# Kernel tuning notes

Measured on AMD Instinct MI355X. Metric: run time of the kernel, lower is better.

## Reference

```python
import jax, jax.numpy as jnp
import numpy as np

DIM = 768
HEADS = 12
HEAD_DIM = DIM // HEADS
R = 8            # LoRA rank (cfg.EXPERT_LOW_RANK)
E = 4            # number of routed LoRA experts in proj (cfg.EXPERT_NUM)
LORA_SCALE = 1.0 / R   # lora_alpha(=1) / r
TOPK_T_PCT = 50  # cfg.topk_tempalte (percent)
TOPK_S_PCT = 25  # cfg.topk_search (percent)
B = 4
N_M = 256        # template / memory tokens
N_S = 1024       # search tokens
N = N_M + N_S
MEM = 1280       # cached memory kv length


def setup_inputs() -> dict:
    key = jax.random.key(0)
    ks = jax.random.split(key, 24)
    g = lambda i, shape: jax.random.normal(ks[i], shape, dtype=jnp.float32) * 0.02
    return dict(
        x=jax.random.normal(ks[0], (B, N, DIM), dtype=jnp.float32),
        id_total=jax.random.normal(ks[1], (B, N_M, DIM), dtype=jnp.float32),
        mem_k=jax.random.normal(ks[2], (B, HEADS, MEM, HEAD_DIM), dtype=jnp.float32),
        mem_v=jax.random.normal(ks[3], (B, HEADS, MEM, HEAD_DIM), dtype=jnp.float32),
        W_qkv=g(4, (3 * DIM, DIM)), b_qkv=g(5, (3 * DIM,)),
        qkv_A=g(6, (3, R, DIM)), qkv_B=g(7, (3, DIM, R)),
        W_proj=g(8, (DIM, DIM)), b_proj=g(9, (DIM,)),
        route_W=g(10, (E, DIM)), proj_A=g(11, (E, R, DIM)), proj_B=g(12, (E, DIM, R)),
        W_idk=g(13, (HEADS, DIM)), b_idk=g(14, (HEADS,)),
        idk_A=g(15, (R, DIM)), idk_B=g(16, (HEADS, R)),
        W_idv=g(17, (DIM, DIM)), b_idv=g(18, (DIM,)),
        idv_A=g(19, (R, DIM)), idv_B=g(20, (DIM, R)),
    )


def _lora1(x, W, b, A, Bm):
    # LinearExperts with lora_num=1: softmax over a single route logit == 1.0
    return x @ W.T + b + ((x @ A.T) @ Bm.T) * LORA_SCALE


def _softmax_w_top(att, top):
    # topk values (sorted desc) -> stable exp relative to the max -> normalize -> scatter
    vals, idx = jax.lax.top_k(att, top)
    e = jnp.exp(vals - vals[..., :1])
    e = e / jnp.sum(e, axis=-1, keepdims=True)
    b, h, q, _ = att.shape
    bi = jnp.arange(b)[:, None, None, None]
    hi = jnp.arange(h)[None, :, None, None]
    qi = jnp.arange(q)[None, None, :, None]
    return jnp.zeros_like(att).at[bi, hi, qi, idx].set(e.astype(att.dtype))


def _forward(x, id_total, mem_k, mem_v, W_qkv, b_qkv, qkv_A, qkv_B,
             W_proj, b_proj, route_W, proj_A, proj_B,
             W_idk, b_idk, idk_A, idk_B, W_idv, b_idv, idv_A, idv_B):
    Bb, Nn, C = x.shape
    Nm = id_total.shape[1]
    Ns = Nn - Nm
    H, D = HEADS, C // HEADS
    # MergedLinear qkv: dense + per-group (q,k,v) LoRA
    low = jnp.einsum('bnc,grc->bngr', x, qkv_A)
    lora = (jnp.einsum('bngr,gcr->bngc', low, qkv_B) * LORA_SCALE).reshape(Bb, Nn, 3 * C)
    qkv = (x @ W_qkv.T + b_qkv + lora).reshape(Bb, Nn, 3, H, D).transpose(2, 0, 3, 1, 4)
    q, k, v = qkv[0], qkv[1], qkv[2]          # each (B,H,N,D)
    k_m, v_m, v_s = k[:, :, :Nm], v[:, :, :Nm], v[:, :, Nm:]
    # memory-token ID gating (id_add=True path)
    ID_K = _lora1(id_total, W_idk, b_idk, idk_A, idk_B)   # (B,Nm,H)
    ID_V = _lora1(id_total, W_idv, b_idv, idv_A, idv_B)   # (B,Nm,C)
    k_m_id = k_m * (1.0 + jnp.tanh(ID_K)).transpose(0, 2, 1)[..., None]
    v_m_flat = v_m.transpose(0, 2, 1, 3).reshape(Bb, Nm, C) + ID_V
    v_m_id = v_m_flat.reshape(Bb, Nm, H, D).transpose(0, 2, 1, 3)
    v_add_id = jnp.concatenate([v_m_id, v_s], axis=2)
    q = q * (D ** -0.5)
    q_m, q_s = q[:, :, :Nm], q[:, :, Nm:]
    # template self-attention with topk softmax
    attn_m = q_m @ k_m_id.transpose(0, 1, 3, 2)           # (B,H,Nm,Nm)
    attn_m = _softmax_w_top(attn_m, int(TOPK_T_PCT / 100 * Nm))
    x_m = (attn_m @ v_m_id).transpose(0, 2, 1, 3).reshape(Bb, Nm, C)
    # search attention over [mem_k, k] (k is the ORIGINAL un-gated key, as in torch)
    k_full = jnp.concatenate([mem_k, k], axis=2)
    v_full = jnp.concatenate([mem_v, v_add_id], axis=2)
    attn_s = q_s @ k_full.transpose(0, 1, 3, 2)           # (B,H,Ns,MEM+N)
    attn_s = _softmax_w_top(attn_s, int(TOPK_S_PCT / 100 * k_full.shape[2]))
    x_s = (attn_s @ v_full).transpose(0, 2, 1, 3).reshape(Bb, Ns, C)
    xo = jnp.concatenate([x_m, x_s], axis=1)
    # LinearExperts proj: dense + softmax-routed LoRA experts
    route = jax.nn.softmax((xo @ route_W.T).astype(jnp.float32), axis=-1).astype(xo.dtype)
    low = jnp.einsum('bnc,erc->bner', xo, proj_A)
    up = jnp.einsum('bner,ecr->bnec', low, proj_B)
    out = xo @ W_proj.T + b_proj + jnp.einsum('bne,bnec->bnc', route, up) * LORA_SCALE
    return out, k_m_id, v_m_id


def reference(x, id_total, mem_k, mem_v, W_qkv, b_qkv, qkv_A, qkv_B,
              W_proj, b_proj, route_W, proj_A, proj_B,
              W_idk, b_idk, idk_A, idk_B, W_idv, b_idv, idv_A, idv_B):
    return _forward(x, id_total, mem_k, mem_v, W_qkv, b_qkv, qkv_A, qkv_B,
                    W_proj, b_proj, route_W, proj_A, proj_B,
                    W_idk, b_idk, idk_A, idk_B, W_idv, b_idv, idv_A, idv_B)
```

## Files before the change

### kernel.cpp

```cpp
#include <hip/hip_runtime.h>
#include <cstddef>

#define Bq    4
#define Hh    12
#define Dd    64
#define NNtok 1280
#define DIMc  768
#define KAUG  800
#define NBH   48

typedef __attribute__((ext_vector_type(8))) short bf16x8;
typedef __attribute__((ext_vector_type(4))) float f32x4;

static const size_t OVb   = 0;
static const size_t OXO   = 3932160;
static const size_t OQL   = 7864320;
static const size_t OIDK  = 7987200;
static const size_t OIDV  = 7999488;
static const size_t OLK   = 8785920;
static const size_t OLV   = 8794112;
static const size_t ORD   = 8802304;
static const size_t OPL   = 8822784;
static const size_t OQH   = 8986624;
static const size_t OKFH  = 10952704;
static const size_t OVTH  = 14884864;
static const size_t OKMH  = 18817024;
static const size_t OVMTH = 19210240;
static const size_t OAa   = 19603456;
static const size_t OWa   = 21651456;
static const size_t OWa2  = 22573056;

static const size_t KMID_OFF = 3932160;
static const size_t VMID_OFF = 4718592;

__device__ __forceinline__ unsigned int pk_bf16(float a, float b) {
  unsigned int ua = __float_as_uint(a), ub = __float_as_uint(b);
  ua += 0x7fffu + ((ua >> 16) & 1u);
  ub += 0x7fffu + ((ub >> 16) & 1u);
  return (ua >> 16) | (ub & 0xffff0000u);
}
__device__ __forceinline__ unsigned short bf16_1(float a) {
  unsigned int ua = __float_as_uint(a);
  ua += 0x7fffu + ((ua >> 16) & 1u);
  return (unsigned short)(ua >> 16);
}
__device__ __forceinline__ float bf2f(unsigned int h) {
  return __uint_as_float(h << 16);
}

__global__ __launch_bounds__(256) void prep(
    const float* __restrict__ mem_k, const float* __restrict__ mem_v,
    const float* __restrict__ W_qkv, const float* __restrict__ qkvB,
    const float* __restrict__ W_proj, const float* __restrict__ projB,
    unsigned short* __restrict__ kfh, unsigned short* __restrict__ vth,
    unsigned short* __restrict__ Wa, unsigned short* __restrict__ Wa2)
{
  __shared__ float tl[64][65];
  const int blk = blockIdx.x, t = threadIdx.x;
  if (blk < 1920) {
    size_t idx = ((size_t)blk * 256 + t) * 8;
    int bh = (int)(idx / 81920);
    int r  = (int)(idx % 81920);
    const float* s = mem_k + (size_t)bh * 81920 + r;
    float4 a = *(const float4*)s;
    float4 b = *(const float4*)(s + 4);
    unsigned int* dp = (unsigned int*)(kfh + (size_t)bh * 163840 + r);
    dp[0] = pk_bf16(a.x, a.y); dp[1] = pk_bf16(a.z, a.w);
    dp[2] = pk_bf16(b.x, b.y); dp[3] = pk_bf16(b.z, b.w);
  } else if (blk < 2880) {
    int b2 = blk - 1920;
    int bh = b2 / 20, t0 = (b2 % 20) * 64;
    const float* sb = mem_v + (size_t)bh * 81920 + (size_t)t0 * 64;
#pragma unroll
    for (int p = 0; p < 4; ++p) {
      int flat = p * 256 + t;
      int r = flat >> 4, c4 = (flat & 15) << 2;
      float4 v = *(const float4*)(sb + r * 64 + c4);
      tl[r][c4 + 0] = v.x; tl[r][c4 + 1] = v.y;
      tl[r][c4 + 2] = v.z; tl[r][c4 + 3] = v.w;
    }
    __syncthreads();
    unsigned short* db = vth + (size_t)bh * 163840 + t0;
#pragma unroll
    for (int p = 0; p < 8; ++p) {
      int flat = p * 256 + t;
      int d = flat >> 5, u = flat & 31;
      *(unsigned int*)(db + (size_t)d * 2560 + 2 * u) = pk_bf16(tl[2 * u][d], tl[2 * u + 1][d]);
    }
  } else if (blk < 6480) {
    int idx = (blk - 2880) * 256 + t;
    int row = idx / 400, c = (idx % 400) * 2;
    float a, b;
    if (c < 768) {
      a = W_qkv[(size_t)row * 768 + c]; b = W_qkv[(size_t)row * 768 + c + 1];
    } else {
      int g = row / 768, jj = row % 768;
      int e0 = c - 768, e1 = e0 + 1;
      a = (e0 < 24 && (e0 >> 3) == g) ? qkvB[(size_t)g * 6144 + jj * 8 + (e0 & 7)] * 0.125f : 0.f;
      b = (e1 < 24 && (e1 >> 3) == g) ? qkvB[(size_t)g * 6144 + jj * 8 + (e1 & 7)] * 0.125f : 0.f;
    }
    *(unsigned int*)(Wa + (size_t)row * KAUG + c) = pk_bf16(a, b);
  } else {
    int idx = (blk - 6480) * 256 + t;
    int row = idx / 400, c = (idx % 400) * 2;
    float a, b;
    if (c < 768) {
      a = W_proj[(size_t)row * 768 + c]; b = W_proj[(size_t)row * 768 + c + 1];
    } else {
      int e0 = c - 768, e1 = e0 + 1;
      a = projB[(size_t)(e0 >> 3) * 6144 + row * 8 + (e0 & 7)];
      b = projB[(size_t)(e1 >> 3) * 6144 + row * 8 + (e1 & 7)];
    }
    *(unsigned int*)(Wa2 + (size_t)row * KAUG + c) = pk_bf16(a, b);
  }
}

__global__ __launch_bounds__(256) void dots_fused(
    const float* __restrict__ x, const float* __restrict__ qkvA,
    float* __restrict__ qlow,
    const float* __restrict__ id_tot, const float* __restrict__ idkA,
    const float* __restrict__ idvA, float* __restrict__ lowk,
    float* __restrict__ lowv)
{
  const int wv = threadIdx.x >> 6, ln = threadIdx.x & 63;
  if (blockIdx.x < 1280) {
    size_t row = (size_t)blockIdx.x * 4 + wv;
    const float* s = x + row * DIMc;
    float xr[12];
#pragma unroll
    for (int i = 0; i < 12; ++i) xr[i] = s[ln + i * 64];
    float p[24];
#pragma unroll
    for (int o = 0; o < 24; ++o) {
      const float* m = qkvA + (size_t)o * DIMc;
      float acc = 0.f;
#pragma unroll
      for (int i = 0; i < 12; ++i) acc += xr[i] * m[ln + i * 64];
      p[o] = acc;
    }
#pragma unroll
    for (int off = 32; off; off >>= 1)
#pragma unroll
      for (int o = 0; o < 24; ++o) p[o] += __shfl_xor(p[o], off, 64);
    if (ln == 0) {
#pragma unroll
      for (int o = 0; o < 24; ++o) qlow[row * 24 + o] = p[o];
    }
  } else {
    size_t row = (size_t)(blockIdx.x - 1280) * 4 + wv;
    const float* s = id_tot + row * DIMc;
    float xr[12];
#pragma unroll
    for (int i = 0; i < 12; ++i) xr[i] = s[ln + i * 64];
    float p[16];
#pragma unroll
    for (int o = 0; o < 8; ++o) {
      const float* m1 = idkA + (size_t)o * DIMc;
      const float* m2 = idvA + (size_t)o * DIMc;
      float a1 = 0.f, a2 = 0.f;
#pragma unroll
      for (int i = 0; i < 12; ++i) {
        a1 += xr[i] * m1[ln + i * 64];
        a2 += xr[i] * m2[ln + i * 64];
      }
      p[o] = a1; p[8 + o] = a2;
    }
#pragma unroll
    for (int off = 32; off; off >>= 1)
#pragma unroll
      for (int o = 0; o < 16; ++o) p[o] += __shfl_xor(p[o], off, 64);
    if (ln == 0) {
#pragma unroll
      for (int o = 0; o < 8; ++o) { lowk[row * 8 + o] = p[o]; lowv[row * 8 + o] = p[8 + o]; }
    }
  }
}

__global__ __launch_bounds__(256) void dot_rp(
    const float* __restrict__ xo, const float* __restrict__ routeW,
    const float* __restrict__ projA, float* __restrict__ rd,
    float* __restrict__ plow)
{
  int wv = threadIdx.x >> 6, ln = threadIdx.x & 63;
  size_t row = (size_t)blockIdx.x * 4 + wv;
  const float* s = xo + row * DIMc;
  float xr[12];
#pragma unroll
  for (int i = 0; i < 12; ++i) xr[i] = s[ln + i * 64];
  float pr[4];
#pragma unroll
  for (int o = 0; o < 4; ++o) {
    const float* m = routeW + (size_t)o * DIMc;
    float acc = 0.f;
#pragma unroll
    for (int i = 0; i < 12; ++i) acc += xr[i] * m[ln + i * 64];
    pr[o] = acc;
  }
  float pl[32];
#pragma unroll
  for (int o = 0; o < 32; ++o) {
    const float* m = projA + (size_t)o * DIMc;
    float acc = 0.f;
#pragma unroll
    for (int i = 0; i < 12; ++i) acc += xr[i] * m[ln + i * 64];
    pl[o] = acc;
  }
#pragma unroll
  for (int off = 32; off; off >>= 1) {
#pragma unroll
    for (int o = 0; o < 4; ++o) pr[o] += __shfl_xor(pr[o], off, 64);
#pragma unroll
    for (int o = 0; o < 32; ++o) pl[o] += __shfl_xor(pl[o], off, 64);
  }
  if (ln == 0) {
#pragma unroll
    for (int o = 0; o < 4; ++o) rd[row * 4 + o] = pr[o];
#pragma unroll
    for (int o = 0; o < 32; ++o) plow[row * 32 + o] = pl[o];
  }
}

__global__ __launch_bounds__(256) void idv_idk(
    const float* __restrict__ id_tot,
    const float* __restrict__ W_idv, const float* __restrict__ b_idv,
    const float* __restrict__ lowv, const float* __restrict__ idv_B,
    float* __restrict__ IDV,
    const float* __restrict__ W_idk, const float* __restrict__ b_idk,
    const float* __restrict__ lowk, const float* __restrict__ idk_B,
    float* __restrict__ IDK)
{
  __shared__ alignas(16) float As[16][68];
  __shared__ alignas(16) float Bs[16][68];
  const int blk = blockIdx.x, t = threadIdx.x;
  if (blk < 192) {
    const int tx = t & 15, ty = t >> 4;
    const int bn = (blk % 12) * 64, bm = (blk / 12) * 64;
    const int am = t >> 2, ak = (t & 3) << 2;
    float acc[4][4] = {};
    for (int k0 = 0; k0 < 768; k0 += 16) {
      float4 av = *(const float4*)(id_tot + (size_t)(bm + am) * 768 + k0 + ak);
      float4 bv = *(const float4*)(W_idv + (size_t)(bn + am) * 768 + k0 + ak);
      As[ak + 0][am] = av.x; As[ak + 1][am] = av.y; As[ak + 2][am] = av.z; As[ak + 3][am] = av.w;
      Bs[ak + 0][am] = bv.x; Bs[ak + 1][am] = bv.y; Bs[ak + 2][am] = bv.z; Bs[ak + 3][am] = bv.w;
      __syncthreads();
#pragma unroll
      for (int kk = 0; kk < 16; ++kk) {
        float4 a4 = *(const float4*)&As[kk][ty << 2];
        float4 b4 = *(const float4*)&Bs[kk][tx << 2];
        float ar[4] = { a4.x, a4.y, a4.z, a4.w };
        float br[4] = { b4.x, b4.y, b4.z, b4.w };
#pragma unroll
        for (int i = 0; i < 4; ++i)
#pragma unroll
          for (int j = 0; j < 4; ++j) acc[i][j] += ar[i] * br[j];
      }
      __syncthreads();
    }
#pragma unroll
    for (int i = 0; i < 4; ++i) {
      int mg = bm + (ty << 2) + i;
#pragma unroll
      for (int j = 0; j < 4; ++j) {
        int col = bn + (tx << 2) + j;
        float v = acc[i][j] + b_idv[col];
        float lo = 0.f;
#pragma unroll
        for (int r = 0; r < 8; ++r) lo += lowv[(size_t)mg * 8 + r] * idv_B[(size_t)col * 8 + r];
        IDV[(size_t)mg * 768 + col] = v + lo * 0.125f;
      }
    }
  } else {
    int wv = t >> 6, ln = t & 63;
    size_t row = (size_t)(blk - 192) * 4 + wv;
    const float* s = id_tot + row * DIMc;
    float xr[12];
#pragma unroll
    for (int i = 0; i < 12; ++i) xr[i] = s[ln + i * 64];
    float p[12];
#pragma unroll
    for (int h = 0; h < 12; ++h) {
      const float* m = W_idk + (size_t)h * DIMc;
      float acc = 0.f;
#pragma unroll
      for (int i = 0; i < 12; ++i) acc += xr[i] * m[ln + i * 64];
      p[h] = acc;
    }
#pragma unroll
    for (int off = 32; off; off >>= 1)
#pragma unroll
      for (int h = 0; h < 12; ++h) p[h] += __shfl_xor(p[h], off, 64);
    if (ln == 0) {
#pragma unroll
      for (int h = 0; h < 12; ++h) {
        float lo = 0.f;
#pragma unroll
        for (int r = 0; r < 8; ++r) lo += lowk[row * 8 + r] * idk_B[h * 8 + r];
        IDK[row * Hh + h] = 1.f + tanhf(p[h] + b_idk[h] + lo * 0.125f);
      }
    }
  }
}

__global__ __launch_bounds__(256) void fixup_kernel(
    float* __restrict__ vb, const float* __restrict__ IDK,
    const float* __restrict__ IDV, float* __restrict__ kmid,
    float* __restrict__ vmid, unsigned short* __restrict__ kmh)
{
  int e = blockIdx.x * 256 + threadIdx.x;
  int d  = e & 63;
  int r1 = e >> 6;
  int tt = r1 & 255;
  int r2 = r1 >> 8;
  int h  = r2 % Hh;
  int b  = r2 / Hh;
  float km = kmid[e] * IDK[(size_t)(b * 256 + tt) * Hh + h];
  kmid[e] = km;
  kmh[e] = bf16_1(km);
  size_t src = ((size_t)(b * Hh + h) * NNtok + tt) * Dd + d;
  float vv = vb[src] + IDV[(size_t)(b * 256 + tt) * DIMc + h * 64 + d];
  vb[src] = vv;
  vmid[e] = vv;
}

__global__ __launch_bounds__(256) void transpose_post(
    const float* __restrict__ vb, unsigned short* __restrict__ vth,
    unsigned short* __restrict__ vmth)
{
  __shared__ float tl[64][65];
  const int blk = blockIdx.x, t = threadIdx.x;
  int bh, t0, dstCols, colOfs;
  unsigned short* dstp;
  size_t dstBh;
  if (blk < 960) { bh = blk / 20; t0 = (blk % 20) * 64; dstp = vth; dstBh = 163840; dstCols = 2560; colOfs = 1280; }
  else { int b2 = blk - 960; bh = b2 / 4; t0 = (b2 % 4) * 64; dstp = vmth; dstBh = 16384; dstCols = 256; colOfs = 0; }
  const float* sb = vb + (size_t)bh * 81920 + (size_t)t0 * 64;
#pragma unroll
  for (int p = 0; p < 4; ++p) {
    int flat = p * 256 + t;
    int r = flat >> 4, c4 = (flat & 15) << 2;
    float4 v = *(const float4*)(sb + r * 64 + c4);
    tl[r][c4 + 0] = v.x; tl[r][c4 + 1] = v.y;
    tl[r][c4 + 2] = v.z; tl[r][c4 + 3] = v.w;
  }
  __syncthreads();
  unsigned short* db = dstp + (size_t)bh * dstBh + colOfs + t0;
#pragma unroll
  for (int p = 0; p < 8; ++p) {
    int flat = p * 256 + t;
    int d = flat >> 5, u = flat & 31;
    *(unsigned int*)(db + (size_t)d * dstCols + 2 * u) = pk_bf16(tl[2 * u][d], tl[2 * u + 1][d]);
  }
}

__global__ __launch_bounds__(256) void cast_pack(
    const float* __restrict__ mainp, const float* __restrict__ extra,
    unsigned short* __restrict__ dst, int extraN)
{
  int idx = blockIdx.x * 256 + threadIdx.x;
  int row = idx / 100, c8 = (idx % 100) * 8;
  unsigned int w[4];
  if (c8 < 768) {
    const float* s = mainp + (size_t)row * 768 + c8;
    float4 a = *(const float4*)s;
    float4 b = *(const float4*)(s + 4);
    w[0] = pk_bf16(a.x, a.y); w[1] = pk_bf16(a.z, a.w);
    w[2] = pk_bf16(b.x, b.y); w[3] = pk_bf16(b.z, b.w);
  } else {
    float v[8];
#pragma unroll
    for (int j = 0; j < 8; ++j) {
      int e = c8 - 768 + j;
      v[j] = (e < extraN) ? extra[(size_t)row * extraN + e] : 0.f;
    }
    w[0] = pk_bf16(v[0], v[1]); w[1] = pk_bf16(v[2], v[3]);
    w[2] = pk_bf16(v[4], v[5]); w[3] = pk_bf16(v[6], v[7]);
  }
  *(uint4*)(dst + (size_t)row * KAUG + c8) = make_uint4(w[0], w[1], w[2], w[3]);
}

__global__ __launch_bounds__(256) void cast_pack_proj(
    const float* __restrict__ xo, const float* __restrict__ rd,
    const float* __restrict__ plow, unsigned short* __restrict__ dst)
{
  int idx = blockIdx.x * 256 + threadIdx.x;
  int row = idx / 100, c8 = (idx % 100) * 8;
  unsigned int w[4];
  if (c8 < 768) {
    const float* s = xo + (size_t)row * 768 + c8;
    float4 a = *(const float4*)s;
    float4 b = *(const float4*)(s + 4);
    w[0] = pk_bf16(a.x, a.y); w[1] = pk_bf16(a.z, a.w);
    w[2] = pk_bf16(b.x, b.y); w[3] = pk_bf16(b.z, b.w);
  } else {
    float l0 = rd[row * 4 + 0], l1 = rd[row * 4 + 1], l2 = rd[row * 4 + 2], l3 = rd[row * 4 + 3];
    float m = fmaxf(fmaxf(l0, l1), fmaxf(l2, l3));
    float e0 = __expf(l0 - m), e1 = __expf(l1 - m), e2 = __expf(l2 - m), e3 = __expf(l3 - m);
    float inv = 0.125f / (e0 + e1 + e2 + e3);
    float rt[4] = { e0 * inv, e1 * inv, e2 * inv, e3 * inv };
    float v[8];
#pragma unroll
    for (int j = 0; j < 8; ++j) {
      int e = c8 - 768 + j;
      v[j] = (e < 32) ? rt[e >> 3] * plow[(size_t)row * 32 + e] : 0.f;
    }
    w[0] = pk_bf16(v[0], v[1]); w[1] = pk_bf16(v[2], v[3]);
    w[2] = pk_bf16(v[4], v[5]); w[3] = pk_bf16(v[6], v[7]);
  }
  *(uint4*)(dst + (size_t)row * KAUG + c8) = make_uint4(w[0], w[1], w[2], w[3]);
}

__global__ __launch_bounds__(256) void gemm_mfma(
    const unsigned short* __restrict__ A, const unsigned short* __restrict__ W,
    const float* __restrict__ bias, int mode, float* __restrict__ dst,
    unsigned short* __restrict__ qh, float* __restrict__ kmid,
    float* __restrict__ vb, unsigned short* __restrict__ kfh)
{
  const int t = threadIdx.x, w = t >> 6, l = t & 63;
  const int m = l & 15, quad = l >> 4;
  const int bm = blockIdx.y * 128 + (w >> 1) * 64;
  const int bn = blockIdx.x * 128 + (w & 1) * 64;
  f32x4 acc[4][4] = {};
  const unsigned short* Ab = A + (size_t)(bm + m) * KAUG;
  const unsigned short* Wb = W + (size_t)(bn + m) * KAUG;
  for (int kk = 0; kk < KAUG; kk += 32) {
    bf16x8 af[4], bf[4];
#pragma unroll
    for (int i = 0; i < 4; ++i) af[i] = *(const bf16x8*)(Ab + (size_t)i * 16 * KAUG + kk + quad * 8);
#pragma unroll
    for (int j = 0; j < 4; ++j) bf[j] = *(const bf16x8*)(Wb + (size_t)j * 16 * KAUG + kk + quad * 8);
#pragma unroll
    for (int i = 0; i < 4; ++i)
#pragma unroll
      for (int j = 0; j < 4; ++j)
        acc[i][j] = __builtin_amdgcn_mfma_f32_16x16x32_bf16(af[i], bf[j], acc[i][j], 0, 0, 0);
  }

  float bj[4];
#pragma unroll
  for (int j = 0; j < 4; ++j) bj[j] = bias[bn + j * 16 + m];

  if (mode == 2) {
#pragma unroll
    for (int i = 0; i < 4; ++i)
#pragma unroll
      for (int r = 0; r < 4; ++r) {
        int row = bm + i * 16 + quad * 4 + r;
#pragma unroll
        for (int j = 0; j < 4; ++j)
          dst[(size_t)row * 768 + bn + j * 16 + m] = acc[i][j][r] + bj[j];
      }
    return;
  }
  int g = (blockIdx.x * 128) / DIMc;
#pragma unroll
  for (int j = 0; j < 4; ++j) {
    int col = bn + j * 16 + m;
    int jj = col - g * DIMc, hh = jj >> 6, d = jj & 63;
#pragma unroll
    for (int i = 0; i < 4; ++i)
#pragma unroll
      for (int r = 0; r < 4; ++r) {
        int row = bm + i * 16 + quad * 4 + r;
        int bb = row / NNtok, tt = row % NNtok;
        float v = acc[i][j][r] + bj[j];
        if (g == 0) {
          qh[((size_t)(bb * Hh + hh) * NNtok + tt) * Dd + d] = bf16_1(v * 0.125f);
        } else if (g == 1) {
          kfh[((size_t)(bb * Hh + hh) * 2560 + 1280 + tt) * Dd + d] = bf16_1(v);
          if (tt < 256) kmid[((size_t)(bb * Hh + hh) * 256 + tt) * Dd + d] = v;
        } else {
          vb[((size_t)(bb * Hh + hh) * NNtok + tt) * Dd + d] = v;
        }
      }
  }
}

__device__ __forceinline__ void radix_sel(
    unsigned int* hist, int l, int& kk, int& ceq, unsigned int& bin)
{
  unsigned int h0 = hist[4 * l + 0], h1 = hist[4 * l + 1],
               h2 = hist[4 * l + 2], h3 = hist[4 * l + 3];
  unsigned int s3 = h3, s2 = h2 + s3, s1 = h1 + s2, s0 = h0 + s1;
  unsigned int tsum = s0;
#pragma unroll
  for (int off = 1; off < 64; off <<= 1) {
    unsigned int other = __shfl(tsum, l + off, 64);
    tsum += (l + off < 64) ? other : 0u;
  }
  unsigned int T = tsum - s0;
  unsigned int Sv0 = T + s0, Sv1 = T + s1, Sv2 = T + s2, Sv3 = T + s3, Sv4 = T;
  int fb = -1, fkk = 0, fceq = 0;
  unsigned int ukk = (unsigned int)kk;
  if (Sv0 >= ukk && Sv1 < ukk) { fb = 4 * l + 0; fkk = (int)(ukk - Sv1); fceq = (int)(Sv0 - Sv1); }
  if (Sv1 >= ukk && Sv2 < ukk) { fb = 4 * l + 1; fkk = (int)(ukk - Sv2); fceq = (int)(Sv1 - Sv2); }
  if (Sv2 >= ukk && Sv3 < ukk) { fb = 4 * l + 2; fkk = (int)(ukk - Sv3); fceq = (int)(Sv2 - Sv3); }
  if (Sv3 >= ukk && Sv4 < ukk) { fb = 4 * l + 3; fkk = (int)(ukk - Sv4); fceq = (int)(Sv3 - Sv4); }
  unsigned long long mb = __ballot(fb >= 0);
  int src = __ffsll(mb) - 1;
  bin = (unsigned int)__shfl(fb, src, 64);
  kk  = __shfl(fkk, src, 64);
  ceq = __shfl(fceq, src, 64);
}

template<int NK>
__global__ __launch_bounds__(256, 3) void attn_mfma7(
    const unsigned short* __restrict__ qh,
    const unsigned short* __restrict__ kf,
    const unsigned short* __restrict__ vt,
    int TK, int qrow0, float* __restrict__ xo, int nofs)
{
  constexpr int SCP = NK + 8;
  constexpr int W = NK / 128;
  constexpr int NRB = (NK == 256) ? 32 : 128;
  __shared__ alignas(16) unsigned short sc16[8][SCP];
  __shared__ unsigned int hist8[8][256];
  __shared__ float wavemax[4][8];
  __shared__ float rowinv[8];

  const int t = threadIdx.x, w = t >> 6, l = t & 63;
  const int xcd  = (int)blockIdx.x & 7;
  const int slot = (int)blockIdx.x >> 3;
  const int bh   = xcd * (NBH / 8) + slot / NRB;
  const int rb   = slot % NRB;
  const int b = bh / Hh, h = bh % Hh;
  const int qbase = qrow0 + rb * 8;
  const int m = l & 15, quad = l >> 4;

  bf16x8 aq0 = {0,0,0,0,0,0,0,0}, aq1 = {0,0,0,0,0,0,0,0};
  if (m < 8) {
    const unsigned short* qp = qh + ((size_t)bh * NNtok + qbase + m) * Dd + quad * 8;
    aq0 = *(const bf16x8*)qp;
    aq1 = *(const bf16x8*)(qp + 32);
  }
  float mx[4] = { -3.0e38f, -3.0e38f, -3.0e38f, -3.0e38f };
  constexpr int ITA = NK / 64;
  constexpr int GA = (ITA >= 4) ? 4 : ITA;
  const unsigned short* kpA = kf + (size_t)bh * NK * Dd + (size_t)(w * 16 + m) * Dd + quad * 8;
  bf16x8 kbuf[2][GA][2];
#pragma unroll
  for (int i = 0; i < GA; ++i) {
    kbuf[0][i][0] = *(const bf16x8*)(kpA + (size_t)i * 64 * Dd);
    kbuf[0][i][1] = *(const bf16x8*)(kpA + (size_t)i * 64 * Dd + 32);
  }
  int ab = 0;
  for (int g0 = 0; g0 < ITA; g0 += GA) {
    if (g0 + GA < ITA) {
#pragma unroll
      for (int i = 0; i < GA; ++i) {
        kbuf[1 - ab][i][0] = *(const bf16x8*)(kpA + (size_t)(g0 + GA + i) * 64 * Dd);
        kbuf[1 - ab][i][1] = *(const bf16x8*)(kpA + (size_t)(g0 + GA + i) * 64 * Dd + 32);
      }
    }
#pragma unroll
    for (int i = 0; i < GA; ++i) {
      int n0 = w * 16 + (g0 + i) * 64;
      f32x4 acc = {0.f, 0.f, 0.f, 0.f};
      acc = __builtin_amdgcn_mfma_f32_16x16x32_bf16(aq0, kbuf[ab][i][0], acc, 0, 0, 0);
      acc = __builtin_amdgcn_mfma_f32_16x16x32_bf16(aq1, kbuf[ab][i][1], acc, 0, 0, 0);
      if (quad < 2) {
#pragma unroll
        for (int r = 0; r < 4; ++r) {
          float v = acc[r];
          mx[r] = fmaxf(mx[r], v);
          sc16[quad * 4 + r][n0 + m] = bf16_1(v);
        }
      }
    }
    ab ^= 1;
  }
#pragma unroll
  for (int off = 1; off < 16; off <<= 1)
#pragma unroll
    for (int r = 0; r < 4; ++r) mx[r] = fmaxf(mx[r], __shfl_xor(mx[r], off, 64));
  if (l == 0) {
#pragma unroll
    for (int r = 0; r < 4; ++r) wavemax[w][r] = mx[r];
  }
  if (l == 16) {
#pragma unroll
    for (int r = 0; r < 4; ++r) wavemax[w][4 + r] = mx[r];
  }
  __syncthreads();

  const int r0i = w * 2, r1i = w * 2 + 1;
  unsigned int* sp0 = (unsigned int*)&sc16[r0i][0];
  unsigned int* sp1 = (unsigned int*)&sc16[r1i][0];
  unsigned int* h0 = hist8[r0i];
  unsigned int* h1 = hist8[r1i];
#pragma unroll
  for (int z = 0; z < 4; ++z) { h0[l + z * 64] = 0u; h1[l + z * 64] = 0u; }
  unsigned int kw0[W], kw1[W];
#pragma unroll
  for (int j = 0; j < W; ++j) {
    unsigned int v0 = sp0[j * 64 + l];
    unsigned int v1 = sp1[j * 64 + l];
    v0 = v0 ^ (((v0 >> 15) & 0x00010001u) * 0x7fffu + 0x80008000u);
    v1 = v1 ^ (((v1 >> 15) & 0x00010001u) * 0x7fffu + 0x80008000u);
    kw0[j] = v0; kw1[j] = v1;
    atomicAdd(&h0[(v0 >> 8) & 255u], 1u);
    atomicAdd(&h0[v0 >> 24], 1u);
    atomicAdd(&h1[(v1 >> 8) & 255u], 1u);
    atomicAdd(&h1[v1 >> 24], 1u);
  }
  int kk0 = TK, kk1 = TK;
  int ceq0s, ceq1s;
  unsigned int bin0, bin1;
  radix_sel(h0, l, kk0, ceq0s, bin0);
  radix_sel(h1, l, kk1, ceq1s, bin1);
  const unsigned int pf0 = bin0 << 8, pf1 = bin1 << 8;
  (void)ceq0s; (void)ceq1s;

  auto finish = [&](unsigned int* kwp, unsigned int prefix, int kk, int row,
                    unsigned int* sp) {
    unsigned int* hist = hist8[row];
#pragma unroll
    for (int z = 0; z < 4; ++z) hist[l + z * 64] = 0u;
    const unsigned int pfx8 = prefix >> 8;
#pragma unroll
    for (int j = 0; j < W; ++j) {
      unsigned int k2 = kwp[j];
      unsigned int lo = k2 & 0xFFFFu, hi = k2 >> 16;
      if ((lo >> 8) == pfx8) atomicAdd(&hist[lo & 255u], 1u);
      if ((hi >> 8) == pfx8) atomicAdd(&hist[hi & 255u], 1u);
    }
    unsigned int b2;
    int ceq = 0;
    radix_sel(hist, l, kk, ceq, b2);
    const unsigned int Tkey = prefix | b2;
    const int need = kk;
    if (need < ceq) {
      int seen = 0;
      unsigned long long below = (1ull << l) - 1ull;
#pragma unroll
      for (int j = 0; j < W; ++j) {
        unsigned int k2 = kwp[j];
        bool eq0 = ((k2 & 0xFFFFu) == Tkey);
        bool eq1 = ((k2 >> 16) == Tkey);
        unsigned long long m0 = __ballot(eq0), m1 = __ballot(eq1);
        int bfr = __popcll(m0 & below) + __popcll(m1 & below);
        if (eq0 && (seen + bfr) >= need) kwp[j] &= 0xFFFF0000u;
        if (eq1 && (seen + bfr + (eq0 ? 1 : 0)) >= need) kwp[j] &= 0x0000FFFFu;
        seen += __popcll(m0) + __popcll(m1);
      }
    }
    float rm = fmaxf(fmaxf(wavemax[0][row], wavemax[1][row]),
                     fmaxf(wavemax[2][row], wavemax[3][row]));
    float sum = 0.f;
#pragma unroll
    for (int j = 0; j < W; ++j) {
      unsigned int k2 = kwp[j];
      unsigned int lo = k2 & 0xFFFFu, hi = k2 >> 16;
      unsigned int mm = ((~k2 >> 15) & 0x00010001u) * 0x7fffu + 0x80008000u;
      unsigned int o2 = k2 ^ mm;
      float v0 = bf2f(o2 & 0xFFFFu);
      float v1 = bf2f(o2 >> 16);
      float w0 = (lo >= Tkey) ? __expf(v0 - rm) : 0.f;
      float w1 = (hi >= Tkey) ? __expf(v1 - rm) : 0.f;
      sp[j * 64 + l] = pk_bf16(w0, w1);
      sum += w0 + w1;
    }
#pragma unroll
    for (int off = 32; off; off >>= 1) sum += __shfl_xor(sum, off, 64);
    if (l == 0) rowinv[row] = 1.f / sum;
  };
  finish(kw0, pf0, kk0, r0i, sp0);
  finish(kw1, pf1, kk1, r1i, sp1);
  __syncthreads();

  constexpr int ITD = NK / 32;
  constexpr int GD = (ITD >= 4) ? 4 : ITD;
  const unsigned short* vrow = vt + (size_t)bh * Dd * NK + (size_t)(w * 16 + m) * NK + quad * 8;
  f32x4 o = {0.f, 0.f, 0.f, 0.f};
  const bf16x8 zz = {0,0,0,0,0,0,0,0};
  bf16x8 vbuf[2][GD], wbuf[2][GD];
#pragma unroll
  for (int i = 0; i < GD; ++i) {
    vbuf[0][i] = *(const bf16x8*)(vrow + i * 32);
    wbuf[0][i] = (m < 8) ? *(const bf16x8*)&sc16[m][i * 32 + quad * 8] : zz;
  }
  int db = 0;
  for (int g0 = 0; g0 < ITD; g0 += GD) {
    if (g0 + GD < ITD) {
#pragma unroll
      for (int i = 0; i < GD; ++i) {
        vbuf[1 - db][i] = *(const bf16x8*)(vrow + (g0 + GD + i) * 32);
        wbuf[1 - db][i] = (m < 8) ? *(const bf16x8*)&sc16[m][(g0 + GD + i) * 32 + quad * 8] : zz;
      }
    }
#pragma unroll
    for (int i = 0; i < GD; ++i)
      o = __builtin_amdgcn_mfma_f32_16x16x32_bf16(wbuf[db][i], vbuf[db][i], o, 0, 0, 0);
    db ^= 1;
  }
  if (quad < 2) {
#pragma unroll
    for (int r = 0; r < 4; ++r) {
      int row = quad * 4 + r;
      int n = nofs + rb * 8 + row;
      xo[((size_t)b * NNtok + n) * DIMc + h * 64 + w * 16 + m] = o[r] * rowinv[row];
    }
  }
}

extern "C" void kernel_launch(void* const* d_in, const int* in_sizes, int n_in,
                              void* d_out, int out_size, void* d_ws, size_t ws_size,
                              hipStream_t stream)
{
  const float* x       = (const float*)d_in[0];
  const float* id_tot  = (const float*)d_in[1];
  const float* mem_k   = (const float*)d_in[2];
  const float* mem_v   = (const float*)d_in[3];
  const float* W_qkv   = (const float*)d_in[4];
  const float* b_qkv   = (const float*)d_in[5];
  const float* qkv_A   = (const float*)d_in[6];
  const float* qkv_B   = (const float*)d_in[7];
  const float* W_proj  = (const float*)d_in[8];
  const float* b_proj  = (const float*)d_in[9];
  const float* route_W = (const float*)d_in[10];
  const float* proj_A  = (const float*)d_in[11];
  const float* proj_B  = (const float*)d_in[12];
  const float* W_idk   = (const float*)d_in[13];
  const float* b_idk   = (const float*)d_in[14];
  const float* idk_A   = (const float*)d_in[15];
  const float* idk_B   = (const float*)d_in[16];
  const float* W_idv   = (const float*)d_in[17];
  const float* b_idv   = (const float*)d_in[18];
  const float* idv_A   = (const float*)d_in[19];
  const float* idv_B   = (const float*)d_in[20];

  float* ws   = (float*)d_ws;
  float* vb   = ws + OVb;
  float* xo   = ws + OXO;
  float* qlow = ws + OQL;
  float* IDK  = ws + OIDK;
  float* IDV  = ws + OIDV;
  float* lowk = ws + OLK;
  float* lowv = ws + OLV;
  float* rd   = ws + ORD;
  float* plow = ws + OPL;
  unsigned short* qh   = (unsigned short*)(ws + OQH);
  unsigned short* kfh  = (unsigned short*)(ws + OKFH);
  unsigned short* vth  = (unsigned short*)(ws + OVTH);
  unsigned short* kmh  = (unsigned short*)(ws + OKMH);
  unsigned short* vmth = (unsigned short*)(ws + OVMTH);
  unsigned short* Aa   = (unsigned short*)(ws + OAa);
  unsigned short* Wa   = (unsigned short*)(ws + OWa);
  unsigned short* Wa2  = (unsigned short*)(ws + OWa2);

  float* out  = (float*)d_out;
  float* kmid = out + KMID_OFF;
  float* vmid = out + VMID_OFF;

  prep<<<7680, 256, 0, stream>>>(mem_k, mem_v, W_qkv, qkv_B, W_proj, proj_B,
                                 kfh, vth, Wa, Wa2);

  dots_fused<<<1536, 256, 0, stream>>>(x, qkv_A, qlow,
                                       id_tot, idk_A, idv_A, lowk, lowv);

  cast_pack<<<2000, 256, 0, stream>>>(x, qlow, Aa, 24);
  gemm_mfma<<<dim3(18, 40), 256, 0, stream>>>(Aa, Wa, b_qkv, 0, nullptr,
                                              qh, kmid, vb, kfh);
  idv_idk<<<448, 256, 0, stream>>>(id_tot, W_idv, b_idv, lowv, idv_B, IDV,
                                   W_idk, b_idk, lowk, idk_B, IDK);
  fixup_kernel<<<3072, 256, 0, stream>>>(vb, IDK, IDV, kmid, vmid, kmh);

  transpose_post<<<1152, 256, 0, stream>>>(vb, vth, vmth);

  attn_mfma7<256><<<1536, 256, 0, stream>>>(qh, kmh, vmth, 128, 0, xo, 0);
  attn_mfma7<2560><<<6144, 256, 0, stream>>>(qh, kfh, vth, 640, 256, xo, 256);

  dot_rp<<<1280, 256, 0, stream>>>(xo, route_W, proj_A, rd, plow);
  cast_pack_proj<<<2000, 256, 0, stream>>>(xo, rd, plow, Aa);
  gemm_mfma<<<dim3(6, 40), 256, 0, stream>>>(Aa, Wa2, b_proj, 2, out,
                                             nullptr, nullptr, nullptr, nullptr);
}
```

Before: 907.2 us.

## Fuse prep with low-rank dots, merge attention launches, fuse routing into proj pack

The low-rank dot products for qkv/id LoRA become extra block ranges of the prep kernel. The two attention launches (memory part and full-context part) become one launch that dispatches on block index, with shared buffers sized for the larger variant. The route/proj_A dot kernel is folded into cast_pack_proj, so the softmax routing and LoRA low values stay in registers instead of going through workspace. The aim is fewer launches, less tail idle between them, and one fewer global round trip. The cost is that the short-context attention blocks now reserve the larger shared allocation, and each wave in the proj pack writes its row serially.

```diff
diff --git a/kernel.cpp b/kernel.cpp
--- a/kernel.cpp
+++ b/kernel.cpp
@@ -19,8 +19,6 @@
 static const size_t OIDV  = 7999488;
 static const size_t OLK   = 8785920;
 static const size_t OLV   = 8794112;
-static const size_t ORD   = 8802304;
-static const size_t OPL   = 8822784;
 static const size_t OQH   = 8986624;
 static const size_t OKFH  = 10952704;
 static const size_t OVTH  = 14884864;
@@ -53,7 +51,12 @@
     const float* __restrict__ W_qkv, const float* __restrict__ qkvB,
     const float* __restrict__ W_proj, const float* __restrict__ projB,
     unsigned short* __restrict__ kfh, unsigned short* __restrict__ vth,
-    unsigned short* __restrict__ Wa, unsigned short* __restrict__ Wa2)
+    unsigned short* __restrict__ Wa, unsigned short* __restrict__ Wa2,
+    const float* __restrict__ x, const float* __restrict__ qkvA,
+    float* __restrict__ qlow,
+    const float* __restrict__ id_tot, const float* __restrict__ idkA,
+    const float* __restrict__ idvA, float* __restrict__ lowk,
+    float* __restrict__ lowv)
 {
   __shared__ float tl[64][65];
   const int blk = blockIdx.x, t = threadIdx.x;
@@ -100,7 +103,7 @@
       b = (e1 < 24 && (e1 >> 3) == g) ? qkvB[(size_t)g * 6144 + jj * 8 + (e1 & 7)] * 0.125f : 0.f;
     }
     *(unsigned int*)(Wa + (size_t)row * KAUG + c) = pk_bf16(a, b);
-  } else {
+  } else if (blk < 7680) {
     int idx = (blk - 6480) * 256 + t;
     int row = idx / 400, c = (idx % 400) * 2;
     float a, b;
@@ -112,111 +115,60 @@
       b = projB[(size_t)(e1 >> 3) * 6144 + row * 8 + (e1 & 7)];
     }
     *(unsigned int*)(Wa2 + (size_t)row * KAUG + c) = pk_bf16(a, b);
-  }
-}
-
-__global__ __launch_bounds__(256) void dots_fused(
-    const float* __restrict__ x, const float* __restrict__ qkvA,
-    float* __restrict__ qlow,
-    const float* __restrict__ id_tot, const float* __restrict__ idkA,
-    const float* __restrict__ idvA, float* __restrict__ lowk,
-    float* __restrict__ lowv)
-{
-  const int wv = threadIdx.x >> 6, ln = threadIdx.x & 63;
-  if (blockIdx.x < 1280) {
-    size_t row = (size_t)blockIdx.x * 4 + wv;
-    const float* s = x + row * DIMc;
-    float xr[12];
-#pragma unroll
-    for (int i = 0; i < 12; ++i) xr[i] = s[ln + i * 64];
-    float p[24];
-#pragma unroll
-    for (int o = 0; o < 24; ++o) {
-      const float* m = qkvA + (size_t)o * DIMc;
-      float acc = 0.f;
-#pragma unroll
-      for (int i = 0; i < 12; ++i) acc += xr[i] * m[ln + i * 64];
-      p[o] = acc;
-    }
-#pragma unroll
-    for (int off = 32; off; off >>= 1)
-#pragma unroll
-      for (int o = 0; o < 24; ++o) p[o] += __shfl_xor(p[o], off, 64);
-    if (ln == 0) {
-#pragma unroll
-      for (int o = 0; o < 24; ++o) qlow[row * 24 + o] = p[o];
-    }
   } else {
-    size_t row = (size_t)(blockIdx.x - 1280) * 4 + wv;
-    const float* s = id_tot + row * DIMc;
-    float xr[12];
-#pragma unroll
-    for (int i = 0; i < 12; ++i) xr[i] = s[ln + i * 64];
-    float p[16];
-#pragma unroll
-    for (int o = 0; o < 8; ++o) {
-      const float* m1 = idkA + (size_t)o * DIMc;
-      const float* m2 = idvA + (size_t)o * DIMc;
-      float a1 = 0.f, a2 = 0.f;
-#pragma unroll
-      for (int i = 0; i < 12; ++i) {
-        a1 += xr[i] * m1[ln + i * 64];
-        a2 += xr[i] * m2[ln + i * 64];
-      }
-      p[o] = a1; p[8 + o] = a2;
-    }
-#pragma unroll
-    for (int off = 32; off; off >>= 1)
-#pragma unroll
-      for (int o = 0; o < 16; ++o) p[o] += __shfl_xor(p[o], off, 64);
-    if (ln == 0) {
-#pragma unroll
-      for (int o = 0; o < 8; ++o) { lowk[row * 8 + o] = p[o]; lowv[row * 8 + o] = p[8 + o]; }
-    }
-  }
-}
-
-__global__ __launch_bounds__(256) void dot_rp(
-    const float* __restrict__ xo, const float* __restrict__ routeW,
-    const float* __restrict__ projA, float* __restrict__ rd,
-    float* __restrict__ plow)
-{
-  int wv = threadIdx.x >> 6, ln = threadIdx.x & 63;
-  size_t row = (size_t)blockIdx.x * 4 + wv;
-  const float* s = xo + row * DIMc;
-  float xr[12];
-#pragma unroll
-  for (int i = 0; i < 12; ++i) xr[i] = s[ln + i * 64];
-  float pr[4];
-#pragma unroll
-  for (int o = 0; o < 4; ++o) {
-    const float* m = routeW + (size_t)o * DIMc;
-    float acc = 0.f;
-#pragma unroll
-    for (int i = 0; i < 12; ++i) acc += xr[i] * m[ln + i * 64];
-    pr[o] = acc;
-  }
-  float pl[32];
-#pragma unroll
-  for (int o = 0; o < 32; ++o) {
-    const float* m = projA + (size_t)o * DIMc;
-    float acc = 0.f;
-#pragma unroll
-    for (int i = 0; i < 12; ++i) acc += xr[i] * m[ln + i * 64];
-    pl[o] = acc;
-  }
-#pragma unroll
-  for (int off = 32; off; off >>= 1) {
-#pragma unroll
-    for (int o = 0; o < 4; ++o) pr[o] += __shfl_xor(pr[o], off, 64);
-#pragma unroll
-    for (int o = 0; o < 32; ++o) pl[o] += __shfl_xor(pl[o], off, 64);
-  }
-  if (ln == 0) {
-#pragma unroll
-    for (int o = 0; o < 4; ++o) rd[row * 4 + o] = pr[o];
-#pragma unroll
-    for (int o = 0; o < 32; ++o) plow[row * 32 + o] = pl[o];
+    const int wv = t >> 6, ln = t & 63;
+    int b2 = blk - 7680;
+    if (b2 < 1280) {
+      size_t row = (size_t)b2 * 4 + wv;
+      const float* s = x + row * DIMc;
+      float xr[12];
+#pragma unroll
+      for (int i = 0; i < 12; ++i) xr[i] = s[ln + i * 64];
+      float p[24];
+#pragma unroll
+      for (int o = 0; o < 24; ++o) {
+        const float* m = qkvA + (size_t)o * DIMc;
+        float acc = 0.f;
+#pragma unroll
+        for (int i = 0; i < 12; ++i) acc += xr[i] * m[ln + i * 64];
+        p[o] = acc;
+      }
+#pragma unroll
+      for (int off = 32; off; off >>= 1)
+#pragma unroll
+        for (int o = 0; o < 24; ++o) p[o] += __shfl_xor(p[o], off, 64);
+      if (ln == 0) {
+#pragma unroll
+        for (int o = 0; o < 24; ++o) qlow[row * 24 + o] = p[o];
+      }
+    } else {
+      size_t row = (size_t)(b2 - 1280) * 4 + wv;
+      const float* s = id_tot + row * DIMc;
+      float xr[12];
+#pragma unroll
+      for (int i = 0; i < 12; ++i) xr[i] = s[ln + i * 64];
+      float p[16];
+#pragma unroll
+      for (int o = 0; o < 8; ++o) {
+        const float* m1 = idkA + (size_t)o * DIMc;
+        const float* m2 = idvA + (size_t)o * DIMc;
+        float a1 = 0.f, a2 = 0.f;
+#pragma unroll
+        for (int i = 0; i < 12; ++i) {
+          a1 += xr[i] * m1[ln + i * 64];
+          a2 += xr[i] * m2[ln + i * 64];
+        }
+        p[o] = a1; p[8 + o] = a2;
+      }
+#pragma unroll
+      for (int off = 32; off; off >>= 1)
+#pragma unroll
+        for (int o = 0; o < 16; ++o) p[o] += __shfl_xor(p[o], off, 64);
+      if (ln == 0) {
+#pragma unroll
+        for (int o = 0; o < 8; ++o) { lowk[row * 8 + o] = p[o]; lowv[row * 8 + o] = p[8 + o]; }
+      }
+    }
   }
 }
 
@@ -379,34 +331,67 @@
 }
 
 __global__ __launch_bounds__(256) void cast_pack_proj(
-    const float* __restrict__ xo, const float* __restrict__ rd,
-    const float* __restrict__ plow, unsigned short* __restrict__ dst)
-{
-  int idx = blockIdx.x * 256 + threadIdx.x;
-  int row = idx / 100, c8 = (idx % 100) * 8;
-  unsigned int w[4];
-  if (c8 < 768) {
-    const float* s = xo + (size_t)row * 768 + c8;
-    float4 a = *(const float4*)s;
-    float4 b = *(const float4*)(s + 4);
-    w[0] = pk_bf16(a.x, a.y); w[1] = pk_bf16(a.z, a.w);
-    w[2] = pk_bf16(b.x, b.y); w[3] = pk_bf16(b.z, b.w);
-  } else {
-    float l0 = rd[row * 4 + 0], l1 = rd[row * 4 + 1], l2 = rd[row * 4 + 2], l3 = rd[row * 4 + 3];
-    float m = fmaxf(fmaxf(l0, l1), fmaxf(l2, l3));
-    float e0 = __expf(l0 - m), e1 = __expf(l1 - m), e2 = __expf(l2 - m), e3 = __expf(l3 - m);
-    float inv = 0.125f / (e0 + e1 + e2 + e3);
-    float rt[4] = { e0 * inv, e1 * inv, e2 * inv, e3 * inv };
-    float v[8];
-#pragma unroll
-    for (int j = 0; j < 8; ++j) {
-      int e = c8 - 768 + j;
-      v[j] = (e < 32) ? rt[e >> 3] * plow[(size_t)row * 32 + e] : 0.f;
-    }
-    w[0] = pk_bf16(v[0], v[1]); w[1] = pk_bf16(v[2], v[3]);
-    w[2] = pk_bf16(v[4], v[5]); w[3] = pk_bf16(v[6], v[7]);
-  }
-  *(uint4*)(dst + (size_t)row * KAUG + c8) = make_uint4(w[0], w[1], w[2], w[3]);
+    const float* __restrict__ xo, const float* __restrict__ routeW,
+    const float* __restrict__ projA, unsigned short* __restrict__ dst)
+{
+  const int wv = threadIdx.x >> 6, ln = threadIdx.x & 63;
+  size_t row = (size_t)blockIdx.x * 4 + wv;
+  const float* s = xo + row * DIMc;
+  float xr[12];
+#pragma unroll
+  for (int i = 0; i < 12; ++i) xr[i] = s[ln + i * 64];
+  float pr[4];
+#pragma unroll
+  for (int o = 0; o < 4; ++o) {
+    const float* m = routeW + (size_t)o * DIMc;
+    float acc = 0.f;
+#pragma unroll
+    for (int i = 0; i < 12; ++i) acc += xr[i] * m[ln + i * 64];
+    pr[o] = acc;
+  }
+  float pl[32];
+#pragma unroll
+  for (int o = 0; o < 32; ++o) {
+    const float* m = projA + (size_t)o * DIMc;
+    float acc = 0.f;
+#pragma unroll
+    for (int i = 0; i < 12; ++i) acc += xr[i] * m[ln + i * 64];
+    pl[o] = acc;
+  }
+#pragma unroll
+  for (int off = 32; off; off >>= 1) {
+#pragma unroll
+    for (int o = 0; o < 4; ++o) pr[o] += __shfl_xor(pr[o], off, 64);
+#pragma unroll
+    for (int o = 0; o < 32; ++o) pl[o] += __shfl_xor(pl[o], off, 64);
+  }
+  float mx = fmaxf(fmaxf(pr[0], pr[1]), fmaxf(pr[2], pr[3]));
+  float e0 = __expf(pr[0] - mx), e1 = __expf(pr[1] - mx),
+        e2 = __expf(pr[2] - mx), e3 = __expf(pr[3] - mx);
+  float inv = 0.125f / (e0 + e1 + e2 + e3);
+  float rt[4] = { e0 * inv, e1 * inv, e2 * inv, e3 * inv };
+  unsigned short* drow = dst + row * KAUG;
+  for (int g = ln; g < 100; g += 64) {
+    int c8 = g * 8;
+    unsigned int w[4];
+    if (c8 < 768) {
+      const float* p = s + c8;
+      float4 a = *(const float4*)p;
+      float4 b = *(const float4*)(p + 4);
+      w[0] = pk_bf16(a.x, a.y); w[1] = pk_bf16(a.z, a.w);
+      w[2] = pk_bf16(b.x, b.y); w[3] = pk_bf16(b.z, b.w);
+    } else {
+      float v[8];
+#pragma unroll
+      for (int j = 0; j < 8; ++j) {
+        int e = c8 - 768 + j;
+        v[j] = (e < 32) ? rt[e >> 3] * pl[e] : 0.f;
+      }
+      w[0] = pk_bf16(v[0], v[1]); w[1] = pk_bf16(v[2], v[3]);
+      w[2] = pk_bf16(v[4], v[5]); w[3] = pk_bf16(v[6], v[7]);
+    }
+    *(uint4*)(drow + c8) = make_uint4(w[0], w[1], w[2], w[3]);
+  }
 }
 
 __global__ __launch_bounds__(256) void gemm_mfma(
@@ -503,23 +488,22 @@
 }
 
 template<int NK>
-__global__ __launch_bounds__(256, 3) void attn_mfma7(
+__device__ __forceinline__ void attn_body(
+    int blk,
     const unsigned short* __restrict__ qh,
     const unsigned short* __restrict__ kf,
     const unsigned short* __restrict__ vt,
-    int TK, int qrow0, float* __restrict__ xo, int nofs)
+    int TK, int qrow0, float* __restrict__ xo, int nofs,
+    unsigned short* __restrict__ scb, unsigned int* __restrict__ histb,
+    float* __restrict__ wavemaxb, float* __restrict__ rowinv)
 {
   constexpr int SCP = NK + 8;
   constexpr int W = NK / 128;
   constexpr int NRB = (NK == 256) ? 32 : 128;
-  __shared__ alignas(16) unsigned short sc16[8][SCP];
-  __shared__ unsigned int hist8[8][256];
-  __shared__ float wavemax[4][8];
-  __shared__ float rowinv[8];
 
   const int t = threadIdx.x, w = t >> 6, l = t & 63;
-  const int xcd  = (int)blockIdx.x & 7;
-  const int slot = (int)blockIdx.x >> 3;
+  const int xcd  = blk & 7;
+  const int slot = blk >> 3;
   const int bh   = xcd * (NBH / 8) + slot / NRB;
   const int rb   = slot % NRB;
   const int b = bh / Hh, h = bh % Hh;
@@ -562,7 +546,7 @@
         for (int r = 0; r < 4; ++r) {
           float v = acc[r];
           mx[r] = fmaxf(mx[r], v);
-          sc16[quad * 4 + r][n0 + m] = bf16_1(v);
+          scb[(quad * 4 + r) * SCP + n0 + m] = bf16_1(v);
         }
       }
     }
@@ -574,19 +558,19 @@
     for (int r = 0; r < 4; ++r) mx[r] = fmaxf(mx[r], __shfl_xor(mx[r], off, 64));
   if (l == 0) {
 #pragma unroll
-    for (int r = 0; r < 4; ++r) wavemax[w][r] = mx[r];
+    for (int r = 0; r < 4; ++r) wavemaxb[w * 8 + r] = mx[r];
   }
   if (l == 16) {
 #pragma unroll
-    for (int r = 0; r < 4; ++r) wavemax[w][4 + r] = mx[r];
+    for (int r = 0; r < 4; ++r) wavemaxb[w * 8 + 4 + r] = mx[r];
   }
   __syncthreads();
 
   const int r0i = w * 2, r1i = w * 2 + 1;
-  unsigned int* sp0 = (unsigned int*)&sc16[r0i][0];
-  unsigned int* sp1 = (unsigned int*)&sc16[r1i][0];
-  unsigned int* h0 = hist8[r0i];
-  unsigned int* h1 = hist8[r1i];
+  unsigned int* sp0 = (unsigned int*)(scb + r0i * SCP);
+  unsigned int* sp1 = (unsigned int*)(scb + r1i * SCP);
+  unsigned int* h0 = histb + r0i * 256;
+  unsigned int* h1 = histb + r1i * 256;
 #pragma unroll
   for (int z = 0; z < 4; ++z) { h0[l + z * 64] = 0u; h1[l + z * 64] = 0u; }
   unsigned int kw0[W], kw1[W];
@@ -612,7 +596,7 @@
 
   auto finish = [&](unsigned int* kwp, unsigned int prefix, int kk, int row,
                     unsigned int* sp) {
-    unsigned int* hist = hist8[row];
+    unsigned int* hist = histb + row * 256;
 #pragma unroll
     for (int z = 0; z < 4; ++z) hist[l + z * 64] = 0u;
     const unsigned int pfx8 = prefix >> 8;
@@ -643,8 +627,8 @@
         seen += __popcll(m0) + __popcll(m1);
       }
     }
-    float rm = fmaxf(fmaxf(wavemax[0][row], wavemax[1][row]),
-                     fmaxf(wavemax[2][row], wavemax[3][row]));
+    float rm = fmaxf(fmaxf(wavemaxb[0 * 8 + row], wavemaxb[1 * 8 + row]),
+                     fmaxf(wavemaxb[2 * 8 + row], wavemaxb[3 * 8 + row]));
     float sum = 0.f;
 #pragma unroll
     for (int j = 0; j < W; ++j) {
@@ -676,7 +660,7 @@
 #pragma unroll
   for (int i = 0; i < GD; ++i) {
     vbuf[0][i] = *(const bf16x8*)(vrow + i * 32);
-    wbuf[0][i] = (m < 8) ? *(const bf16x8*)&sc16[m][i * 32 + quad * 8] : zz;
+    wbuf[0][i] = (m < 8) ? *(const bf16x8*)(scb + m * SCP + i * 32 + quad * 8) : zz;
   }
   int db = 0;
   for (int g0 = 0; g0 < ITD; g0 += GD) {
@@ -684,7 +668,7 @@
 #pragma unroll
       for (int i = 0; i < GD; ++i) {
         vbuf[1 - db][i] = *(const bf16x8*)(vrow + (g0 + GD + i) * 32);
-        wbuf[1 - db][i] = (m < 8) ? *(const bf16x8*)&sc16[m][(g0 + GD + i) * 32 + quad * 8] : zz;
+        wbuf[1 - db][i] = (m < 8) ? *(const bf16x8*)(scb + m * SCP + (g0 + GD + i) * 32 + quad * 8) : zz;
       }
     }
 #pragma unroll
@@ -699,6 +683,25 @@
       int n = nofs + rb * 8 + row;
       xo[((size_t)b * NNtok + n) * DIMc + h * 64 + w * 16 + m] = o[r] * rowinv[row];
     }
+  }
+}
+
+__global__ __launch_bounds__(256, 3) void attn_fused(
+    const unsigned short* __restrict__ qh,
+    const unsigned short* __restrict__ kfh, const unsigned short* __restrict__ vth,
+    const unsigned short* __restrict__ kmh, const unsigned short* __restrict__ vmth,
+    float* __restrict__ xo)
+{
+  __shared__ alignas(16) unsigned short sc_raw[8 * 2568];
+  __shared__ unsigned int hist_raw[8 * 256];
+  __shared__ float wm_raw[32];
+  __shared__ float ri_raw[8];
+  if (blockIdx.x < 6144) {
+    attn_body<2560>((int)blockIdx.x, qh, kfh, vth, 640, 256, xo, 256,
+                    sc_raw, hist_raw, wm_raw, ri_raw);
+  } else {
+    attn_body<256>((int)blockIdx.x - 6144, qh, kmh, vmth, 128, 0, xo, 0,
+                   sc_raw, hist_raw, wm_raw, ri_raw);
   }
 }
 
@@ -736,8 +739,6 @@
   float* IDV  = ws + OIDV;
   float* lowk = ws + OLK;
   float* lowv = ws + OLV;
-  float* rd   = ws + ORD;
-  float* plow = ws + OPL;
   unsigned short* qh   = (unsigned short*)(ws + OQH);
   unsigned short* kfh  = (unsigned short*)(ws + OKFH);
   unsigned short* vth  = (unsigned short*)(ws + OVTH);
@@ -751,11 +752,9 @@
   float* kmid = out + KMID_OFF;
   float* vmid = out + VMID_OFF;
 
-  prep<<<7680, 256, 0, stream>>>(mem_k, mem_v, W_qkv, qkv_B, W_proj, proj_B,
-                                 kfh, vth, Wa, Wa2);
-
-  dots_fused<<<1536, 256, 0, stream>>>(x, qkv_A, qlow,
-                                       id_tot, idk_A, idv_A, lowk, lowv);
+  prep<<<9216, 256, 0, stream>>>(mem_k, mem_v, W_qkv, qkv_B, W_proj, proj_B,
+                                 kfh, vth, Wa, Wa2,
+                                 x, qkv_A, qlow, id_tot, idk_A, idv_A, lowk, lowv);
 
   cast_pack<<<2000, 256, 0, stream>>>(x, qlow, Aa, 24);
   gemm_mfma<<<dim3(18, 40), 256, 0, stream>>>(Aa, Wa, b_qkv, 0, nullptr,
@@ -766,11 +765,9 @@
 
   transpose_post<<<1152, 256, 0, stream>>>(vb, vth, vmth);
 
-  attn_mfma7<256><<<1536, 256, 0, stream>>>(qh, kmh, vmth, 128, 0, xo, 0);
-  attn_mfma7<2560><<<6144, 256, 0, stream>>>(qh, kfh, vth, 640, 256, xo, 256);
-
-  dot_rp<<<1280, 256, 0, stream>>>(xo, route_W, proj_A, rd, plow);
-  cast_pack_proj<<<2000, 256, 0, stream>>>(xo, rd, plow, Aa);
+  attn_fused<<<7680, 256, 0, stream>>>(qh, kfh, vth, kmh, vmth, xo);
+
+  cast_pack_proj<<<1280, 256, 0, stream>>>(xo, route_W, proj_A, Aa);
   gemm_mfma<<<dim3(6, 40), 256, 0, stream>>>(Aa, Wa2, b_proj, 2, out,
                                              nullptr, nullptr, nullptr, nullptr);
 }
```

New measurement: 812.3 us. 1.12x faster.
